# Performance work log

Measured on AMD Instinct MI355X. Metric: run time of the kernel, lower is better.

Reference implementation:

```python
import jax, jax.numpy as jnp
import numpy as np

N_NODES = 100000
N_EDGES = 1600000
IN_SIZE = 128
HIDDEN = 128
OUT_SIZE = 64


def setup_inputs() -> dict:
    key = jax.random.key(0)
    k = jax.random.split(key, 8)
    feat = jax.random.normal(k[0], (N_NODES, IN_SIZE), dtype=jnp.float32)
    src = jax.random.randint(k[1], (N_EDGES,), 0, N_NODES, dtype=jnp.int32)
    dst = jax.random.randint(k[2], (N_EDGES,), 0, N_NODES, dtype=jnp.int32)
    # fc_neigh weights for the two SAGEConv layers (stored as [in, out])
    W1 = jax.random.normal(k[3], (IN_SIZE, HIDDEN), dtype=jnp.float32) / np.sqrt(IN_SIZE)
    b1 = jnp.zeros((HIDDEN,), dtype=jnp.float32)
    W2 = jax.random.normal(k[4], (HIDDEN, OUT_SIZE), dtype=jnp.float32) / np.sqrt(HIDDEN)
    b2 = jnp.zeros((OUT_SIZE,), dtype=jnp.float32)
    return {"feat": feat, "W1": W1, "b1": b1, "W2": W2, "b2": b2,
            "src": src, "dst": dst}


def _sage_gcn(h, src, dst, W, b):
    # DGL SAGEConv with aggregator_type='gcn':
    #   neigh = segment_sum over incoming edges of src features
    #   h_neigh = (neigh + h_self) / (in_degree + 1)
    #   out = h_neigh @ W + b   (fc_self is not used for 'gcn')
    neigh = jax.ops.segment_sum(h[src], dst, num_segments=N_NODES)  # [N, d]
    deg = jax.ops.segment_sum(jnp.ones((src.shape[0],), dtype=h.dtype), dst,
                              num_segments=N_NODES)                 # [N]
    h_neigh = (neigh + h) / (deg + 1.0)[:, None]
    return h_neigh @ W + b


def reference(feat, W1, b1, W2, b2, src, dst):
    # dropout(p=0.0) is identity; activation between layers only
    h = _sage_gcn(feat, src, dst, W1, b1)
    h = jax.nn.relu(h)
    h = _sage_gcn(h, src, dst, W2, b2)
    return h
```

## Files before the change

kernel.cpp:

```cpp
#include <hip/hip_runtime.h>

#define NNODES 100000
#define NEDGES 1600000
#define BSHIFT 7
#define NB 782
#define CAP 2560
#define EBLOCKS 391
#define GEMM_BLOCKS 1563

typedef _Float16 f16;
typedef _Float16 v8h __attribute__((ext_vector_type(8)));
typedef float v4f __attribute__((ext_vector_type(4)));

#if __has_builtin(__builtin_amdgcn_cvt_f32_ubyte0)
#define CVTB0(u) __builtin_amdgcn_cvt_f32_ubyte0(u)
#define CVTB1(u) __builtin_amdgcn_cvt_f32_ubyte1(u)
#define CVTB2(u) __builtin_amdgcn_cvt_f32_ubyte2(u)
#define CVTB3(u) __builtin_amdgcn_cvt_f32_ubyte3(u)
#else
#define CVTB0(u) ((float)((u) & 0xFFu))
#define CVTB1(u) ((float)(((u) >> 8) & 0xFFu))
#define CVTB2(u) ((float)(((u) >> 16) & 0xFFu))
#define CVTB3(u) ((float)((u) >> 24))
#endif

__device__ inline void acc8(float s, uint2 u, float* a) {
    a[0] = fmaf(s, CVTB0(u.x), a[0]);
    a[1] = fmaf(s, CVTB1(u.x), a[1]);
    a[2] = fmaf(s, CVTB2(u.x), a[2]);
    a[3] = fmaf(s, CVTB3(u.x), a[3]);
    a[4] = fmaf(s, CVTB0(u.y), a[4]);
    a[5] = fmaf(s, CVTB1(u.y), a[5]);
    a[6] = fmaf(s, CVTB2(u.y), a[6]);
    a[7] = fmaf(s, CVTB3(u.y), a[7]);
}

__global__ __launch_bounds__(256) void init_k(int* __restrict__ bcur,
                                              const float* __restrict__ W1,
                                              f16* __restrict__ W1t,
                                              const float* __restrict__ W2,
                                              f16* __restrict__ W2t) {
    int t = blockIdx.x * 256 + threadIdx.x;
    if (t < NB) bcur[t] = t * CAP;
    int u = t - 1024;
    if (u >= 0) {
        if (u < 128 * 128) {
            int k = u >> 7, n = u & 127;
            W1t[n * 128 + k] = (f16)W1[k * 128 + n];
        } else if (u < 128 * 128 + 128 * 64) {
            int v = u - 128 * 128;
            int k = v >> 6, n = v & 63;
            W2t[n * 128 + k] = (f16)W2[k * 64 + n];
        }
    }
}

__global__ __launch_bounds__(256) void scatter_gemm1(
    const int* __restrict__ src, const int* __restrict__ dst,
    int* __restrict__ bcur, int* __restrict__ ebuf,
    const float* __restrict__ feat, const f16* __restrict__ W1t,
    unsigned char* __restrict__ z1, float* __restrict__ sc1) {
    constexpr int PITCH = 136;
    __shared__ __align__(16) char smem[128 * PITCH * 2];
    int tid = threadIdx.x;

    if (blockIdx.x < EBLOCKS) {
        int* h = (int*)smem;
        int* base_s = ((int*)smem) + 1024;
        for (int i = tid; i < NB; i += 256) h[i] = 0;
        __syncthreads();
        int base = blockIdx.x * 4096;
        int d[16], sv[16];
        for (int k = 0; k < 16; k++) {
            int e = base + k * 256 + tid;
            if (e < NEDGES) {
                d[k] = dst[e];
                sv[k] = src[e];
                atomicAdd(&h[d[k] >> BSHIFT], 1);
            } else {
                d[k] = -1;
            }
        }
        __syncthreads();
        for (int i = tid; i < NB; i += 256) {
            int c = h[i];
            if (c) base_s[i] = atomicAdd(&bcur[i], c);
            h[i] = 0;
        }
        __syncthreads();
        for (int k = 0; k < 16; k++) {
            if (d[k] >= 0) {
                int b = d[k] >> BSHIFT;
                int slot = atomicAdd(&h[b], 1);
                ebuf[base_s[b] + slot] = sv[k] | ((d[k] & 127) << 24);
            }
        }
        return;
    }

    f16* wlds = (f16*)smem;
    for (int c = tid; c < 128 * 16; c += 256) {
        int n = c >> 4;
        int kc = c & 15;
        *(v8h*)&wlds[n * PITCH + kc * 8] = *(const v8h*)&W1t[n * 128 + kc * 8];
    }
    __syncthreads();

    int wave = tid >> 6, lane = tid & 63, quad = lane >> 4, l16 = lane & 15;
    int m0 = (blockIdx.x - EBLOCKS) * 64 + wave * 16;
    if (m0 >= NNODES) return;

    v8h a[4];
    const float* arow = feat + (long)(m0 + l16) * 128 + quad * 8;
#pragma unroll
    for (int kb = 0; kb < 4; kb++) {
        float4 f0 = *(const float4*)(arow + kb * 32);
        float4 f1 = *(const float4*)(arow + kb * 32 + 4);
        v8h t = {(f16)f0.x, (f16)f0.y, (f16)f0.z, (f16)f0.w,
                 (f16)f1.x, (f16)f1.y, (f16)f1.z, (f16)f1.w};
        a[kb] = t;
    }

    v4f acc[8];
#pragma unroll
    for (int nt = 0; nt < 8; nt++) {
        v4f c4 = {0.f, 0.f, 0.f, 0.f};
        const f16* brow = &wlds[(nt * 16 + l16) * PITCH + quad * 8];
#pragma unroll
        for (int kb = 0; kb < 4; kb++) {
            v8h b = *(const v8h*)(brow + kb * 32);
            c4 = __builtin_amdgcn_mfma_f32_16x16x32_f16(a[kb], b, c4, 0, 0, 0);
        }
        acc[nt] = c4;
    }

#pragma unroll
    for (int r = 0; r < 4; r++) {
        float m = 0.f;
#pragma unroll
        for (int nt = 0; nt < 8; nt++) m = fmaxf(m, fabsf(acc[nt][r]));
        m = fmaxf(m, __shfl_xor(m, 1));
        m = fmaxf(m, __shfl_xor(m, 2));
        m = fmaxf(m, __shfl_xor(m, 4));
        m = fmaxf(m, __shfl_xor(m, 8));
        int row = m0 + quad * 4 + r;
        float rs = (m > 0.f) ? 127.f / m : 0.f;
        if (l16 == 0) sc1[row] = (m > 0.f) ? m / 127.f : 0.f;
#pragma unroll
        for (int nt = 0; nt < 8; nt++) {
            int qv = (int)rintf(acc[nt][r] * rs) + 128;
            z1[(long)row * 128 + nt * 16 + l16] = (unsigned char)qv;
        }
    }
}

__global__ __launch_bounds__(256) void fill_bucket(const int* __restrict__ ebuf,
                                                   const int* __restrict__ bcur,
                                                   const float* __restrict__ sc1,
                                                   int* __restrict__ begs,
                                                   int* __restrict__ ends,
                                                   int* __restrict__ csr4,
                                                   int2* __restrict__ csr8) {
    __shared__ int lc[128];
    __shared__ int ls[256];
    int b = blockIdx.x;
    int tid = threadIdx.x;
    if (tid < 128) lc[tid] = 0;
    __syncthreads();
    int ebeg = b * CAP;
    int eend = bcur[b];
    for (int e = ebeg + tid; e < eend; e += 256)
        atomicAdd(&lc[((unsigned)ebuf[e]) >> 24], 1);
    __syncthreads();
    int cnt = (tid < 128) ? lc[tid] : 0;
    ls[tid] = cnt;
    __syncthreads();
    for (int off = 1; off < 256; off <<= 1) {
        int t = (tid >= off) ? ls[tid - off] : 0;
        __syncthreads();
        ls[tid] += t;
        __syncthreads();
    }
    int excl = ls[tid] - cnt;
    int node = (b << BSHIFT) + tid;
    if (tid < 128 && node < NNODES) {
        begs[node] = ebeg + excl;
        ends[node] = ebeg + excl + cnt;
    }
    if (tid < 128) { ls[tid] = excl; lc[tid] = 0; }
    __syncthreads();
    for (int e = ebeg + tid; e < eend; e += 256) {
        int p = ebuf[e];
        int dloc = ((unsigned)p) >> 24;
        int s = p & 0xFFFFFF;
        int slot = atomicAdd(&lc[dloc], 1);
        int pos = ebeg + ls[dloc] + slot;
        csr4[pos] = s;
        csr8[pos] = make_int2(s, __float_as_int(sc1[s]));
    }
}

__global__ __launch_bounds__(1024, 8) void gather128_gemm2(
    const unsigned char* __restrict__ z,
    const float* __restrict__ sc,
    const int2* __restrict__ csr8,
    const int* __restrict__ begs, const int* __restrict__ ends,
    const float* __restrict__ b1,
    const f16* __restrict__ W2t,
    unsigned char* __restrict__ z2,
    float* __restrict__ sc2)
{
    constexpr int PITCH = 136;
    __shared__ f16 w2lds[64 * PITCH];
    __shared__ f16 atile[64 * PITCH];
    __shared__ int rmax[64];
    int tid = threadIdx.x;

    {
        int n = tid >> 4, kc = tid & 15;
        *(v8h*)&w2lds[n * PITCH + kc * 8] = *(const v8h*)&W2t[n * 128 + kc * 8];
    }
    if (tid < 64) rmax[tid] = 0;

    int wavei = tid >> 6;
    int lane = tid & 63;
    int sub = lane >> 4;
    int c = lane & 15;
    int lnode = wavei * 4 + sub;
    int node = blockIdx.x * 64 + lnode;

    int beg = 0, end = 0;
    if (node < NNODES) { beg = begs[node]; end = ends[node]; }

    unsigned coff = (unsigned)c << 3;

    float a[8];
#pragma unroll
    for (int j = 0; j < 8; j++) a[j] = 0.f;
    float ssum = 0.f;

    if (node < NNODES) {
        float s = sc[node];
        uint2 u = *(const uint2*)(z + (((unsigned)node) << 7) + coff);
        ssum += s;
        acc8(s, u, a);
    }

    int e = beg;
    while (__any(e < end)) {
        int2 q0 = {0, 0}, q1 = {0, 0}, q2 = {0, 0}, q3 = {0, 0};
        int2 q4 = {0, 0}, q5 = {0, 0}, q6 = {0, 0}, q7 = {0, 0};
        if (e     < end) q0 = csr8[e];
        if (e + 1 < end) q1 = csr8[e + 1];
        if (e + 2 < end) q2 = csr8[e + 2];
        if (e + 3 < end) q3 = csr8[e + 3];
        if (e + 4 < end) q4 = csr8[e + 4];
        if (e + 5 < end) q5 = csr8[e + 5];
        if (e + 6 < end) q6 = csr8[e + 6];
        if (e + 7 < end) q7 = csr8[e + 7];
        uint2 u0 = make_uint2(0, 0), u1 = make_uint2(0, 0);
        uint2 u2 = make_uint2(0, 0), u3 = make_uint2(0, 0);
        uint2 u4 = make_uint2(0, 0), u5 = make_uint2(0, 0);
        uint2 u6 = make_uint2(0, 0), u7 = make_uint2(0, 0);
        if (e     < end) u0 = *(const uint2*)(z + (((unsigned)q0.x) << 7) + coff);
        if (e + 1 < end) u1 = *(const uint2*)(z + (((unsigned)q1.x) << 7) + coff);
        if (e + 2 < end) u2 = *(const uint2*)(z + (((unsigned)q2.x) << 7) + coff);
        if (e + 3 < end) u3 = *(const uint2*)(z + (((unsigned)q3.x) << 7) + coff);
        if (e + 4 < end) u4 = *(const uint2*)(z + (((unsigned)q4.x) << 7) + coff);
        if (e + 5 < end) u5 = *(const uint2*)(z + (((unsigned)q5.x) << 7) + coff);
        if (e + 6 < end) u6 = *(const uint2*)(z + (((unsigned)q6.x) << 7) + coff);
        if (e + 7 < end) u7 = *(const uint2*)(z + (((unsigned)q7.x) << 7) + coff);
        float s0 = __int_as_float(q0.y), s1 = __int_as_float(q1.y);
        float s2 = __int_as_float(q2.y), s3 = __int_as_float(q3.y);
        float s4 = __int_as_float(q4.y), s5 = __int_as_float(q5.y);
        float s6 = __int_as_float(q6.y), s7 = __int_as_float(q7.y);
        ssum += ((s0 + s1) + (s2 + s3)) + ((s4 + s5) + (s6 + s7));
        acc8(s0, u0, a); acc8(s1, u1, a); acc8(s2, u2, a); acc8(s3, u3, a);
        acc8(s4, u4, a); acc8(s5, u5, a); acc8(s6, u6, a); acc8(s7, u7, a);
        e += 8;
    }

    {
        float base = 128.f * ssum;
        float inv = 1.0f / (float)(end - beg + 1);
        float4 bb0 = ((const float4*)b1)[c * 2];
        float4 bb1 = ((const float4*)b1)[c * 2 + 1];
        v8h o = {(f16)fmaxf((a[0] - base) * inv + bb0.x, 0.f),
                 (f16)fmaxf((a[1] - base) * inv + bb0.y, 0.f),
                 (f16)fmaxf((a[2] - base) * inv + bb0.z, 0.f),
                 (f16)fmaxf((a[3] - base) * inv + bb0.w, 0.f),
                 (f16)fmaxf((a[4] - base) * inv + bb1.x, 0.f),
                 (f16)fmaxf((a[5] - base) * inv + bb1.y, 0.f),
                 (f16)fmaxf((a[6] - base) * inv + bb1.z, 0.f),
                 (f16)fmaxf((a[7] - base) * inv + bb1.w, 0.f)};
        *(v8h*)&atile[lnode * PITCH + c * 8] = o;
    }
    __syncthreads();

    {
        int wr = wavei >> 2, wc = wavei & 3;
        int quad = lane >> 4, l16 = lane & 15;
        const f16* arow = &atile[(wr * 16 + l16) * PITCH + quad * 8];
        const f16* brow = &w2lds[(wc * 16 + l16) * PITCH + quad * 8];
        v4f acc = {0.f, 0.f, 0.f, 0.f};
#pragma unroll
        for (int kb = 0; kb < 4; kb++) {
            v8h av = *(const v8h*)(arow + kb * 32);
            v8h bv = *(const v8h*)(brow + kb * 32);
            acc = __builtin_amdgcn_mfma_f32_16x16x32_f16(av, bv, acc, 0, 0, 0);
        }
#pragma unroll
        for (int r = 0; r < 4; r++) {
            float m = fabsf(acc[r]);
            m = fmaxf(m, __shfl_xor(m, 1));
            m = fmaxf(m, __shfl_xor(m, 2));
            m = fmaxf(m, __shfl_xor(m, 4));
            m = fmaxf(m, __shfl_xor(m, 8));
            if (l16 == 0) atomicMax(&rmax[wr * 16 + quad * 4 + r], __float_as_int(m));
        }
        __syncthreads();
#pragma unroll
        for (int r = 0; r < 4; r++) {
            int lrow = wr * 16 + quad * 4 + r;
            int row = blockIdx.x * 64 + lrow;
            if (row < NNODES) {
                float m = __int_as_float(rmax[lrow]);
                float rs = (m > 0.f) ? 127.f / m : 0.f;
                int qv = (int)rintf(acc[r] * rs) + 128;
                z2[(long)row * 64 + wc * 16 + l16] = (unsigned char)qv;
                if (l16 == 0 && wc == 0) sc2[row] = (m > 0.f) ? m / 127.f : 0.f;
            }
        }
    }
}

__global__ __launch_bounds__(256, 8) void gather64(
    const unsigned char* __restrict__ z, const float* __restrict__ sc,
    const int* __restrict__ begs, const int* __restrict__ ends,
    const int* __restrict__ csr,
    const float* __restrict__ bias, float4* __restrict__ out) {
    int tid = threadIdx.x;
    int lane = tid & 63;
    int c = lane & 7;
    int node = blockIdx.x * 32 + (tid >> 3);

    int beg = begs[node];
    int end = ends[node];

    unsigned coff = (unsigned)c << 3;

    float a[8];
#pragma unroll
    for (int j = 0; j < 8; j++) a[j] = 0.f;
    float ssum = 0.f;

    {
        float s = sc[node];
        uint2 u = *(const uint2*)(z + (((unsigned)node) << 6) + coff);
        ssum += s;
        acc8(s, u, a);
    }

    int e = beg;
    while (__any(e < end)) {
        float s0 = 0.f, s1 = 0.f, s2 = 0.f, s3 = 0.f;
        float s4 = 0.f, s5 = 0.f, s6 = 0.f, s7 = 0.f;
        uint2 u0 = make_uint2(0, 0), u1 = make_uint2(0, 0);
        uint2 u2 = make_uint2(0, 0), u3 = make_uint2(0, 0);
        uint2 u4 = make_uint2(0, 0), u5 = make_uint2(0, 0);
        uint2 u6 = make_uint2(0, 0), u7 = make_uint2(0, 0);
        if (e     < end) { int i = csr[e    ]; s0 = sc[i]; u0 = *(const uint2*)(z + (((unsigned)i) << 6) + coff); }
        if (e + 1 < end) { int i = csr[e + 1]; s1 = sc[i]; u1 = *(const uint2*)(z + (((unsigned)i) << 6) + coff); }
        if (e + 2 < end) { int i = csr[e + 2]; s2 = sc[i]; u2 = *(const uint2*)(z + (((unsigned)i) << 6) + coff); }
        if (e + 3 < end) { int i = csr[e + 3]; s3 = sc[i]; u3 = *(const uint2*)(z + (((unsigned)i) << 6) + coff); }
        if (e + 4 < end) { int i = csr[e + 4]; s4 = sc[i]; u4 = *(const uint2*)(z + (((unsigned)i) << 6) + coff); }
        if (e + 5 < end) { int i = csr[e + 5]; s5 = sc[i]; u5 = *(const uint2*)(z + (((unsigned)i) << 6) + coff); }
        if (e + 6 < end) { int i = csr[e + 6]; s6 = sc[i]; u6 = *(const uint2*)(z + (((unsigned)i) << 6) + coff); }
        if (e + 7 < end) { int i = csr[e + 7]; s7 = sc[i]; u7 = *(const uint2*)(z + (((unsigned)i) << 6) + coff); }
        ssum += ((s0 + s1) + (s2 + s3)) + ((s4 + s5) + (s6 + s7));
        acc8(s0, u0, a); acc8(s1, u1, a); acc8(s2, u2, a); acc8(s3, u3, a);
        acc8(s4, u4, a); acc8(s5, u5, a); acc8(s6, u6, a); acc8(s7, u7, a);
        e += 8;
    }

    {
        float base = 128.f * ssum;
        float inv = 1.0f / (float)(end - beg + 1);
        float4 b0 = ((const float4*)bias)[c * 2];
        float4 b1v = ((const float4*)bias)[c * 2 + 1];
        out[(long)node * 16 + c * 2] =
            make_float4((a[0] - base) * inv + b0.x, (a[1] - base) * inv + b0.y,
                        (a[2] - base) * inv + b0.z, (a[3] - base) * inv + b0.w);
        out[(long)node * 16 + c * 2 + 1] =
            make_float4((a[4] - base) * inv + b1v.x, (a[5] - base) * inv + b1v.y,
                        (a[6] - base) * inv + b1v.z, (a[7] - base) * inv + b1v.w);
    }
}

extern "C" void kernel_launch(void* const* d_in, const int* in_sizes, int n_in,
                              void* d_out, int out_size, void* d_ws, size_t ws_size,
                              hipStream_t stream) {
    const float* feat = (const float*)d_in[0];
    const float* W1   = (const float*)d_in[1];
    const float* b1   = (const float*)d_in[2];
    const float* W2   = (const float*)d_in[3];
    const float* b2   = (const float*)d_in[4];
    const int*   src  = (const int*)d_in[5];
    const int*   dst  = (const int*)d_in[6];
    float* out = (float*)d_out;

    char* ws = (char*)d_ws;
    int* bcur = (int*)(ws + 0x0000000);
    int* begs = (int*)(ws + 0x0001000);
    int* ends = (int*)(ws + 0x0063000);
    int* ebuf = (int*)(ws + 0x00C5000);
    int* csr4 = (int*)(ws + 0x0900000);
    int2* csr8 = (int2*)(ws + 0x1100000);
    unsigned char* z1 = (unsigned char*)(ws + 0x2100000);
    float* sc1 = (float*)(ws + 0x2E00000);
    unsigned char* z2 = (unsigned char*)(ws + 0x2F00000);
    float* sc2 = (float*)(ws + 0x3600000);
    f16* W1t  = (f16*)(ws + 0x3700000);
    f16* W2t  = (f16*)(ws + 0x3710000);

    init_k<<<100, 256, 0, stream>>>(bcur, W1, W1t, W2, W2t);

    scatter_gemm1<<<EBLOCKS + GEMM_BLOCKS, 256, 0, stream>>>(src, dst, bcur, ebuf,
                                                             feat, W1t, z1, sc1);

    fill_bucket<<<NB, 256, 0, stream>>>(ebuf, bcur, sc1, begs, ends, csr4, csr8);

    gather128_gemm2<<<1563, 1024, 0, stream>>>(z1, sc1, csr8, begs, ends, b1, W2t,
                                               z2, sc2);

    gather64<<<3125, 256, 0, stream>>>(z2, sc2, begs, ends, csr4, b2, (float4*)out);
}
```

Baseline: 261.1 us.

## Split fused layer-1 gather and GEMM2 into separate kernels, drop csr4

The fused 1024-thread gather+GEMM2 kernel is split in two. A 256-thread gather kernel writes the fp16 layer-1 activations to a global buffer, and a separate MFMA GEMM kernel quantizes the result to int8 with per-row scales. The separate int-only CSR array is removed, so gather64 now reads the source index from the 8-byte csr8 entries. The aim is to free the gather from block-wide syncs and heavy LDS use and to cut one CSR write, at the cost of an extra global round-trip for h1 and wider index reads in gather64.

```diff
diff --git a/kernel.cpp b/kernel.cpp
--- a/kernel.cpp
+++ b/kernel.cpp
@@ -159,7 +159,6 @@
                                                    const float* __restrict__ sc1,
                                                    int* __restrict__ begs,
                                                    int* __restrict__ ends,
-                                                   int* __restrict__ csr4,
                                                    int2* __restrict__ csr8) {
     __shared__ int lc[128];
     __shared__ int ls[256];
@@ -194,43 +193,24 @@
         int dloc = ((unsigned)p) >> 24;
         int s = p & 0xFFFFFF;
         int slot = atomicAdd(&lc[dloc], 1);
-        int pos = ebeg + ls[dloc] + slot;
-        csr4[pos] = s;
-        csr8[pos] = make_int2(s, __float_as_int(sc1[s]));
-    }
-}
-
-__global__ __launch_bounds__(1024, 8) void gather128_gemm2(
+        csr8[ebeg + ls[dloc] + slot] = make_int2(s, __float_as_int(sc1[s]));
+    }
+}
+
+__global__ __launch_bounds__(256, 8) void gather128_h1(
     const unsigned char* __restrict__ z,
     const float* __restrict__ sc,
     const int2* __restrict__ csr8,
     const int* __restrict__ begs, const int* __restrict__ ends,
     const float* __restrict__ b1,
-    const f16* __restrict__ W2t,
-    unsigned char* __restrict__ z2,
-    float* __restrict__ sc2)
+    f16* __restrict__ h1)
 {
-    constexpr int PITCH = 136;
-    __shared__ f16 w2lds[64 * PITCH];
-    __shared__ f16 atile[64 * PITCH];
-    __shared__ int rmax[64];
     int tid = threadIdx.x;
-
-    {
-        int n = tid >> 4, kc = tid & 15;
-        *(v8h*)&w2lds[n * PITCH + kc * 8] = *(const v8h*)&W2t[n * 128 + kc * 8];
-    }
-    if (tid < 64) rmax[tid] = 0;
-
-    int wavei = tid >> 6;
-    int lane = tid & 63;
-    int sub = lane >> 4;
-    int c = lane & 15;
-    int lnode = wavei * 4 + sub;
-    int node = blockIdx.x * 64 + lnode;
-
-    int beg = 0, end = 0;
-    if (node < NNODES) { beg = begs[node]; end = ends[node]; }
+    int c = tid & 15;
+    int node = blockIdx.x * 16 + (tid >> 4);
+
+    int beg = begs[node];
+    int end = ends[node];
 
     unsigned coff = (unsigned)c << 3;
 
@@ -239,7 +219,7 @@
     for (int j = 0; j < 8; j++) a[j] = 0.f;
     float ssum = 0.f;
 
-    if (node < NNODES) {
+    {
         float s = sc[node];
         uint2 u = *(const uint2*)(z + (((unsigned)node) << 7) + coff);
         ssum += s;
@@ -293,51 +273,72 @@
                  (f16)fmaxf((a[5] - base) * inv + bb1.y, 0.f),
                  (f16)fmaxf((a[6] - base) * inv + bb1.z, 0.f),
                  (f16)fmaxf((a[7] - base) * inv + bb1.w, 0.f)};
-        *(v8h*)&atile[lnode * PITCH + c * 8] = o;
-    }
-    __syncthreads();
-
-    {
-        int wr = wavei >> 2, wc = wavei & 3;
-        int quad = lane >> 4, l16 = lane & 15;
-        const f16* arow = &atile[(wr * 16 + l16) * PITCH + quad * 8];
-        const f16* brow = &w2lds[(wc * 16 + l16) * PITCH + quad * 8];
-        v4f acc = {0.f, 0.f, 0.f, 0.f};
+        *(v8h*)&h1[(long)node * 128 + c * 8] = o;
+    }
+}
+
+__global__ __launch_bounds__(256) void gemm2_k(
+    const f16* __restrict__ h1,
+    const f16* __restrict__ W2t,
+    unsigned char* __restrict__ z2,
+    float* __restrict__ sc2)
+{
+    constexpr int PITCH = 136;
+    __shared__ f16 wlds[64 * PITCH];
+    int tid = threadIdx.x;
+    for (int c = tid; c < 64 * 16; c += 256) {
+        int n = c >> 4;
+        int kc = c & 15;
+        *(v8h*)&wlds[n * PITCH + kc * 8] = *(const v8h*)&W2t[n * 128 + kc * 8];
+    }
+    __syncthreads();
+
+    int wave = tid >> 6, lane = tid & 63, quad = lane >> 4, l16 = lane & 15;
+    int m0 = blockIdx.x * 64 + wave * 16;
+    if (m0 >= NNODES) return;
+
+    v8h a[4];
+    const f16* arow = h1 + (long)(m0 + l16) * 128 + quad * 8;
+#pragma unroll
+    for (int kb = 0; kb < 4; kb++) a[kb] = *(const v8h*)(arow + kb * 32);
+
+    v4f acc[4];
+#pragma unroll
+    for (int nt = 0; nt < 4; nt++) {
+        v4f c4 = {0.f, 0.f, 0.f, 0.f};
+        const f16* brow = &wlds[(nt * 16 + l16) * PITCH + quad * 8];
 #pragma unroll
         for (int kb = 0; kb < 4; kb++) {
-            v8h av = *(const v8h*)(arow + kb * 32);
-            v8h bv = *(const v8h*)(brow + kb * 32);
-            acc = __builtin_amdgcn_mfma_f32_16x16x32_f16(av, bv, acc, 0, 0, 0);
-        }
-#pragma unroll
-        for (int r = 0; r < 4; r++) {
-            float m = fabsf(acc[r]);
-            m = fmaxf(m, __shfl_xor(m, 1));
-            m = fmaxf(m, __shfl_xor(m, 2));
-            m = fmaxf(m, __shfl_xor(m, 4));
-            m = fmaxf(m, __shfl_xor(m, 8));
-            if (l16 == 0) atomicMax(&rmax[wr * 16 + quad * 4 + r], __float_as_int(m));
-        }
-        __syncthreads();
-#pragma unroll
-        for (int r = 0; r < 4; r++) {
-            int lrow = wr * 16 + quad * 4 + r;
-            int row = blockIdx.x * 64 + lrow;
-            if (row < NNODES) {
-                float m = __int_as_float(rmax[lrow]);
-                float rs = (m > 0.f) ? 127.f / m : 0.f;
-                int qv = (int)rintf(acc[r] * rs) + 128;
-                z2[(long)row * 64 + wc * 16 + l16] = (unsigned char)qv;
-                if (l16 == 0 && wc == 0) sc2[row] = (m > 0.f) ? m / 127.f : 0.f;
-            }
+            v8h b = *(const v8h*)(brow + kb * 32);
+            c4 = __builtin_amdgcn_mfma_f32_16x16x32_f16(a[kb], b, c4, 0, 0, 0);
+        }
+        acc[nt] = c4;
+    }
+
+#pragma unroll
+    for (int r = 0; r < 4; r++) {
+        float m = 0.f;
+#pragma unroll
+        for (int nt = 0; nt < 4; nt++) m = fmaxf(m, fabsf(acc[nt][r]));
+        m = fmaxf(m, __shfl_xor(m, 1));
+        m = fmaxf(m, __shfl_xor(m, 2));
+        m = fmaxf(m, __shfl_xor(m, 4));
+        m = fmaxf(m, __shfl_xor(m, 8));
+        int row = m0 + quad * 4 + r;
+        float rs = (m > 0.f) ? 127.f / m : 0.f;
+        if (l16 == 0) sc2[row] = (m > 0.f) ? m / 127.f : 0.f;
+#pragma unroll
+        for (int nt = 0; nt < 4; nt++) {
+            int qv = (int)rintf(acc[nt][r] * rs) + 128;
+            z2[(long)row * 64 + nt * 16 + l16] = (unsigned char)qv;
         }
     }
 }
 
 __global__ __launch_bounds__(256, 8) void gather64(
     const unsigned char* __restrict__ z, const float* __restrict__ sc,
+    const int2* __restrict__ csr8,
     const int* __restrict__ begs, const int* __restrict__ ends,
-    const int* __restrict__ csr,
     const float* __restrict__ bias, float4* __restrict__ out) {
     int tid = threadIdx.x;
     int lane = tid & 63;
@@ -369,14 +370,14 @@
         uint2 u2 = make_uint2(0, 0), u3 = make_uint2(0, 0);
         uint2 u4 = make_uint2(0, 0), u5 = make_uint2(0, 0);
         uint2 u6 = make_uint2(0, 0), u7 = make_uint2(0, 0);
-        if (e     < end) { int i = csr[e    ]; s0 = sc[i]; u0 = *(const uint2*)(z + (((unsigned)i) << 6) + coff); }
-        if (e + 1 < end) { int i = csr[e + 1]; s1 = sc[i]; u1 = *(const uint2*)(z + (((unsigned)i) << 6) + coff); }
-        if (e + 2 < end) { int i = csr[e + 2]; s2 = sc[i]; u2 = *(const uint2*)(z + (((unsigned)i) << 6) + coff); }
-        if (e + 3 < end) { int i = csr[e + 3]; s3 = sc[i]; u3 = *(const uint2*)(z + (((unsigned)i) << 6) + coff); }
-        if (e + 4 < end) { int i = csr[e + 4]; s4 = sc[i]; u4 = *(const uint2*)(z + (((unsigned)i) << 6) + coff); }
-        if (e + 5 < end) { int i = csr[e + 5]; s5 = sc[i]; u5 = *(const uint2*)(z + (((unsigned)i) << 6) + coff); }
-        if (e + 6 < end) { int i = csr[e + 6]; s6 = sc[i]; u6 = *(const uint2*)(z + (((unsigned)i) << 6) + coff); }
-        if (e + 7 < end) { int i = csr[e + 7]; s7 = sc[i]; u7 = *(const uint2*)(z + (((unsigned)i) << 6) + coff); }
+        if (e     < end) { int i = csr8[e    ].x; s0 = sc[i]; u0 = *(const uint2*)(z + (((unsigned)i) << 6) + coff); }
+        if (e + 1 < end) { int i = csr8[e + 1].x; s1 = sc[i]; u1 = *(const uint2*)(z + (((unsigned)i) << 6) + coff); }
+        if (e + 2 < end) { int i = csr8[e + 2].x; s2 = sc[i]; u2 = *(const uint2*)(z + (((unsigned)i) << 6) + coff); }
+        if (e + 3 < end) { int i = csr8[e + 3].x; s3 = sc[i]; u3 = *(const uint2*)(z + (((unsigned)i) << 6) + coff); }
+        if (e + 4 < end) { int i = csr8[e + 4].x; s4 = sc[i]; u4 = *(const uint2*)(z + (((unsigned)i) << 6) + coff); }
+        if (e + 5 < end) { int i = csr8[e + 5].x; s5 = sc[i]; u5 = *(const uint2*)(z + (((unsigned)i) << 6) + coff); }
+        if (e + 6 < end) { int i = csr8[e + 6].x; s6 = sc[i]; u6 = *(const uint2*)(z + (((unsigned)i) << 6) + coff); }
+        if (e + 7 < end) { int i = csr8[e + 7].x; s7 = sc[i]; u7 = *(const uint2*)(z + (((unsigned)i) << 6) + coff); }
         ssum += ((s0 + s1) + (s2 + s3)) + ((s4 + s5) + (s6 + s7));
         acc8(s0, u0, a); acc8(s1, u1, a); acc8(s2, u2, a); acc8(s3, u3, a);
         acc8(s4, u4, a); acc8(s5, u5, a); acc8(s6, u6, a); acc8(s7, u7, a);
@@ -414,24 +415,27 @@
     int* begs = (int*)(ws + 0x0001000);
     int* ends = (int*)(ws + 0x0063000);
     int* ebuf = (int*)(ws + 0x00C5000);
-    int* csr4 = (int*)(ws + 0x0900000);
-    int2* csr8 = (int2*)(ws + 0x1100000);
-    unsigned char* z1 = (unsigned char*)(ws + 0x2100000);
-    float* sc1 = (float*)(ws + 0x2E00000);
-    unsigned char* z2 = (unsigned char*)(ws + 0x2F00000);
-    float* sc2 = (float*)(ws + 0x3600000);
-    f16* W1t  = (f16*)(ws + 0x3700000);
-    f16* W2t  = (f16*)(ws + 0x3710000);
+    int2* csr8 = (int2*)(ws + 0x0900000);
+    unsigned char* z1 = (unsigned char*)(ws + 0x1900000);
+    float* sc1 = (float*)(ws + 0x2600000);
+    f16* h1   = (f16*)(ws + 0x2700000);
+    unsigned char* z2 = (unsigned char*)(ws + 0x4100000);
+    float* sc2 = (float*)(ws + 0x4800000);
+    f16* W1t  = (f16*)(ws + 0x4900000);
+    f16* W2t  = (f16*)(ws + 0x4910000);
 
     init_k<<<100, 256, 0, stream>>>(bcur, W1, W1t, W2, W2t);
 
     scatter_gemm1<<<EBLOCKS + GEMM_BLOCKS, 256, 0, stream>>>(src, dst, bcur, ebuf,
                                                              feat, W1t, z1, sc1);
 
-    fill_bucket<<<NB, 256, 0, stream>>>(ebuf, bcur, sc1, begs, ends, csr4, csr8);
-
-    gather128_gemm2<<<1563, 1024, 0, stream>>>(z1, sc1, csr8, begs, ends, b1, W2t,
-                                               z2, sc2);
-
-    gather64<<<3125, 256, 0, stream>>>(z2, sc2, begs, ends, csr4, b2, (float4*)out);
-}
+    fill_bucket<<<NB, 256, 0, stream>>>(ebuf, bcur, sc1, begs, ends, csr8);
+
+    gather128_h1<<<NNODES / 16, 256, 0, stream>>>(z1, sc1, csr8, begs, ends,
+                                                  b1, h1);
+
+    gemm2_k<<<GEMM_BLOCKS, 256, 0, stream>>>(h1, W2t, z2, sc2);
+
+    gather64<<<3125, 256, 0, stream>>>(z2, sc2, csr8, begs, ends, b2,
+                                       (float4*)out);
+}
```

New measurement: 249.9 us (median of 2 runs). -4.3%, faster.
